# Performance work log

Measured on AMD Instinct MI355X. Metric: run time of the kernel, lower is better.

Reference implementation:

```python
import jax, jax.numpy as jnp
import numpy as np

B, T, IN_DIM = 256, 256, 64
HID, DIM2, OUT_DIM, N_HEADS = 1024, 512, 16, 32


def _linear(x, w, b):
    return x @ w.T + b


def _gru(x, h0, w_ih, w_hh, b_ih, b_hh):
    # x: [B,T,HID], h0: [B,HID]; returns final hidden [B,HID]
    gi_all = jnp.einsum('bti,gi->btg', x, w_ih) + b_ih  # [B,T,3H] precomputed input gates
    def step(h, gi):
        gh = h @ w_hh.T + b_hh
        i_r, i_z, i_n = jnp.split(gi, 3, axis=-1)
        h_r, h_z, h_n = jnp.split(gh, 3, axis=-1)
        r = jax.nn.sigmoid(i_r + h_r)
        z = jax.nn.sigmoid(i_z + h_z)
        n = jnp.tanh(i_n + r * h_n)
        h_new = (1.0 - z) * n + z * h
        return h_new, None
    h, _ = jax.lax.scan(step, h0, jnp.swapaxes(gi_all, 0, 1))
    return h


def setup_inputs() -> dict:
    key = jax.random.key(0)
    ks = jax.random.split(key, 16)
    s = 0.05
    inp = {
        'input': jax.random.normal(ks[0], (B, T, IN_DIM), jnp.float32),
        'hn': jnp.zeros((1, B, HID), jnp.float32),
        'cultivars': jax.random.randint(ks[1], (B, 1), 0, N_HEADS, jnp.int32),
        'fc1_w': jax.random.normal(ks[2], (DIM2, IN_DIM), jnp.float32) * s,
        'fc1_b': jnp.zeros((DIM2,), jnp.float32),
        'fc2_w': jax.random.normal(ks[3], (HID, DIM2), jnp.float32) * s,
        'fc2_b': jnp.zeros((HID,), jnp.float32),
        'w_ih': jax.random.normal(ks[4], (3 * HID, HID), jnp.float32) * s,
        'w_hh': jax.random.normal(ks[5], (3 * HID, HID), jnp.float32) * s,
        'b_ih': jnp.zeros((3 * HID,), jnp.float32),
        'b_hh': jnp.zeros((3 * HID,), jnp.float32),
        'fc3_w': jax.random.normal(ks[6], (DIM2, HID), jnp.float32) * s,
        'fc3_b': jnp.zeros((DIM2,), jnp.float32),
        'heads_w': jax.random.normal(ks[7], (N_HEADS, OUT_DIM, DIM2), jnp.float32) * s,
        'heads_b': jnp.zeros((N_HEADS, OUT_DIM), jnp.float32),
    }
    return inp


def reference(input, hn, cultivars, fc1_w, fc1_b, fc2_w, fc2_b, w_ih, w_hh, b_ih, b_hh, fc3_w, fc3_b, heads_w, heads_b):
    x = _linear(input, fc1_w, fc1_b)          # [B,T,DIM2]
    x = _linear(x, fc2_w, fc2_b)              # [B,T,HID]
    h = _gru(x, hn[0], w_ih, w_hh, b_ih, b_hh)  # [B,HID]
    hn_out = h[None]                          # [1,B,HID]
    out = jax.nn.relu(hn_out)
    out = jax.nn.relu(_linear(out, fc3_w, fc3_b))[0]  # [B,DIM2]
    cidx = cultivars[:, 0]                    # [B]
    w_sel = heads_w[cidx]                     # [B,OUT_DIM,DIM2] gathered head weights
    b_sel = heads_b[cidx]                     # [B,OUT_DIM]
    params = jnp.einsum('bd,bod->bo', out, w_sel) + b_sel
    return params, hn_out
```

## Files before the change

kernel.cpp:

```cpp
#include <hip/hip_runtime.h>

#define T_   256
#define HID_ 1024
#define D2   512

typedef __attribute__((ext_vector_type(8))) short  short8;
typedef __attribute__((ext_vector_type(8))) __bf16 bf16x8;
typedef __attribute__((ext_vector_type(4))) float  f32x4;

__device__ __forceinline__ float sigmoidf_(float x) {
    return __fdividef(1.0f, 1.0f + __expf(-x));
}
__device__ __forceinline__ float tanhf_(float x) {
    return 1.0f - __fdividef(2.0f, 1.0f + __expf(2.0f * x));
}
__device__ __forceinline__ unsigned short bf16hi(float x) {
    unsigned u = __float_as_uint(x);
    return (unsigned short)((u + 0x7FFFu + ((u >> 16) & 1u)) >> 16);
}
__device__ __forceinline__ float bf2f(unsigned short h) {
    return __uint_as_float((unsigned)h << 16);
}
__device__ __forceinline__ f32x4 mfma_(short8 a, short8 b, f32x4 c) {
    union { short8 s; bf16x8 b; } ua, ub;
    ua.s = a; ub.s = b;
    return __builtin_amdgcn_mfma_f32_16x16x32_bf16(ua.b, ub.b, c, 0, 0, 0);
}

__device__ __forceinline__ void gl16(short8& d, const void* p) {
    asm volatile("global_load_dwordx4 %0, %1, off" : "=v"(d) : "v"(p));
}
__device__ __forceinline__ void gl16c(short8& d, const void* p) {
    asm volatile("global_load_dwordx4 %0, %1, off sc0 sc1" : "=v"(d) : "v"(p));
}
__device__ __forceinline__ void gs8c(void* p, unsigned long long v) {
    asm volatile("global_store_dwordx2 %0, %1, off sc0 sc1"
                 :: "v"(p), "v"(v) : "memory");
}
#define WAITV0() asm volatile("s_waitcnt vmcnt(0)" ::: "memory")
#define WAITV8() asm volatile("s_waitcnt vmcnt(8)" ::: "memory")
#define WAITV10_TIE(H, L) asm volatile("s_waitcnt vmcnt(10)" : "+v"(H), "+v"(L) :: "memory")
#define WAITV2_TIE(H, L)  asm volatile("s_waitcnt vmcnt(2)"  : "+v"(H), "+v"(L) :: "memory")
#define WAITV0_TIE(H, L)  asm volatile("s_waitcnt vmcnt(0)"  : "+v"(H), "+v"(L) :: "memory")
#define ABAR() asm volatile("s_waitcnt lgkmcnt(0)\n\ts_barrier" ::: "memory")

__global__ __launch_bounds__(256) void k_w2(
    const float* __restrict__ fc2_w, const float* __restrict__ fc1_w,
    const float* __restrict__ fc1_b, const float* __restrict__ fc2_b,
    float* __restrict__ W2, float* __restrict__ b2)
{
    int idx = blockIdx.x * 256 + threadIdx.x;
    int r = idx >> 6, c = idx & 63;
    float acc = 0.f;
    for (int k = 0; k < D2; ++k)
        acc += fc2_w[(size_t)r * D2 + k] * fc1_w[(size_t)k * 64 + c];
    W2[idx] = acc;
    if (c == 0) {
        float a = fc2_b[r];
        for (int k = 0; k < D2; ++k)
            a += fc2_w[(size_t)r * D2 + k] * fc1_b[k];
        b2[r] = a;
    }
}

__global__ __launch_bounds__(256) void k_wc(
    const float* __restrict__ w_ih, const float* __restrict__ W2,
    const float* __restrict__ b2, const float* __restrict__ b_ih,
    unsigned short* __restrict__ wc_hi, unsigned short* __restrict__ wc_lo,
    float* __restrict__ bc)
{
    int idx = blockIdx.x * 256 + threadIdx.x;
    int r = idx >> 6, c = idx & 63;
    float acc = 0.f;
    for (int k = 0; k < HID_; ++k)
        acc += w_ih[(size_t)r * HID_ + k] * W2[(size_t)k * 64 + c];
    unsigned short h = bf16hi(acc);
    wc_hi[idx] = h;
    wc_lo[idx] = bf16hi(acc - bf2f(h));
    if (c == 0) {
        float a = b_ih[r];
        for (int k = 0; k < HID_; ++k)
            a += w_ih[(size_t)r * HID_ + k] * b2[k];
        bc[r] = a;
    }
}

__global__ __launch_bounds__(256) void k_splitw(
    const float* __restrict__ w, unsigned short* __restrict__ hi,
    unsigned short* __restrict__ lo)
{
    int i4 = (blockIdx.x * 256 + threadIdx.x) * 4;
    float4 v = *(const float4*)(w + i4);
    float vv[4] = {v.x, v.y, v.z, v.w};
    unsigned short h4[4], l4[4];
    #pragma unroll
    for (int i = 0; i < 4; ++i) {
        h4[i] = bf16hi(vv[i]);
        l4[i] = bf16hi(vv[i] - bf2f(h4[i]));
    }
    *(unsigned long long*)(hi + i4) =
        (unsigned long long)h4[0] | ((unsigned long long)h4[1] << 16) |
        ((unsigned long long)h4[2] << 32) | ((unsigned long long)h4[3] << 48);
    *(unsigned long long*)(lo + i4) =
        (unsigned long long)l4[0] | ((unsigned long long)l4[1] << 16) |
        ((unsigned long long)l4[2] << 32) | ((unsigned long long)l4[3] << 48);
}

__global__ __launch_bounds__(256) void k_split_h0(
    const float* __restrict__ hn, unsigned short* __restrict__ hi,
    unsigned short* __restrict__ lo)
{
    int gid = blockIdx.x * 256 + threadIdx.x;
    int b = gid >> 7, kseg = gid & 127;
    const float* src = hn + (size_t)b * HID_ + kseg * 8;
    short8 h8, l8;
    #pragma unroll
    for (int i = 0; i < 8; ++i) {
        float v = src[i];
        unsigned short h = bf16hi(v);
        ((short*)&h8)[i] = (short)h;
        ((short*)&l8)[i] = (short)bf16hi(v - bf2f(h));
    }
    size_t off = (size_t)(kseg >> 2) * 8192 + b * 32 + (kseg & 3) * 8;
    *(short8*)(hi + off) = h8;
    *(short8*)(lo + off) = l8;
}

__global__ __launch_bounds__(256, 1) void k_gru(
    const float* __restrict__ input,
    const float* __restrict__ hn,
    const float* __restrict__ b_hh,
    const float* __restrict__ bc,
    const unsigned short* __restrict__ whh_hi,
    const unsigned short* __restrict__ whh_lo,
    const unsigned short* __restrict__ wc_hi,
    const unsigned short* __restrict__ wc_lo,
    unsigned short* __restrict__ hxA_hi, unsigned short* __restrict__ hxA_lo,
    unsigned short* __restrict__ hxB_hi, unsigned short* __restrict__ hxB_lo,
    float* __restrict__ hn_out,
    int* __restrict__ bar)
{
    const int g = blockIdx.x, ct = g & 31, bt = g >> 5;
    const int j0 = ct << 5, b0 = bt << 5;
    const int tid = threadIdx.x, lane = tid & 63, wid = tid >> 6;
    const int mh = wid & 1, kh = wid >> 1;
    const int l15 = lane & 15, quad = lane >> 4;

    __shared__ short smB[36864];
    float* smF = (float*)smB;
    const int SIN_ = 4672, SHN_ = 6784;

    const int t7 = tid & 127, pl = tid >> 7;
    const unsigned short* wsrc = pl ? whh_lo : whh_hi;
    const unsigned short* csrc = pl ? wc_lo : wc_hi;
    const char* wB[3]; const char* cB[3]; int lo_[3];
    #pragma unroll
    for (int i = 0; i < 3; ++i) {
        int sid = t7 + (i << 7);
        int n = sid >> 2, ss = sid & 3;
        int grow = (n >> 5) * HID_ + j0 + (n & 31);
        wB[i] = (const char*)wsrc + (size_t)grow * 2048u + (size_t)ss * 16u;
        cB[i] = (const char*)csrc + (size_t)grow * 128u + (size_t)ss * 16u;
        lo_[i] = (pl * 96 + n) * 32 + ((ss * 8) ^ (((n >> 1) & 3) << 3));
    }
    const int foff = l15 * 32 + ((quad * 8) ^ (((l15 >> 1) & 3) << 3));
    const size_t aoff = (size_t)((b0 + mh * 16 + l15) * 64 + quad * 16);
    const char* aAh = (const char*)hxA_hi + aoff;
    const char* aAl = (const char*)hxA_lo + aoff;
    const char* aBh = (const char*)hxB_hi + aoff;
    const char* aBl = (const char*)hxB_lo + aoff;
    const float* xrow = input + (size_t)(b0 + mh * 16 + l15) * (T_ * 64)
                              + kh * 32 + quad * 8;

    const int gb = tid >> 3, gj4 = (tid & 7) << 2;
    float hreg[4], br[4], bz[4], bni[4], bnh[4];
    #pragma unroll
    for (int i = 0; i < 4; ++i) {
        int j = j0 + gj4 + i;
        hreg[i] = hn[(size_t)(b0 + gb) * HID_ + j];
        br[i]  = bc[j] + b_hh[j];
        bz[i]  = bc[1024 + j] + b_hh[1024 + j];
        bni[i] = bc[2048 + j];
        bnh[i] = b_hh[2048 + j];
    }
    const size_t hoff = (size_t)(ct * 16384 + (b0 + gb) * 64 + gj4 * 2);
    char* sAh = (char*)hxA_hi + hoff; char* sAl = (char*)hxA_lo + hoff;
    char* sBh = (char*)hxB_hi + hoff; char* sBl = (char*)hxB_lo + hoff;
    const int g73 = gb * 73, g33 = gb * 33;

    int* flags = bar + bt * 128;

    short8 bp[2][6];
    short8 ab[3][2];
    f32x4 acc[6], acci[2];

#define GH_CHUNK(RB, AH, AL)                                                  \
  { _Pragma("unroll")                                                         \
    for (int nt = 0; nt < 6; ++nt) {                                          \
        short8 bh_ = *(const short8*)(smB + (RB) + nt * 512 + foff);          \
        short8 bl_ = *(const short8*)(smB + (RB) + 3072 + nt * 512 + foff);   \
        f32x4 v_ = mfma_(AH, bh_, acc[nt]);                                   \
        v_ = mfma_(AH, bl_, v_);                                              \
        v_ = mfma_(AL, bh_, v_);                                              \
        acc[nt] = v_; } }

    #pragma unroll 1
    for (int t = 0; t < 256; ++t) {
        const char* rh = (t & 1) ? aBh : aAh;
        const char* rl = (t & 1) ? aBl : aAl;
        char* wh = (t & 1) ? sAh : sBh;
        char* wl = (t & 1) ? sAl : sBl;

        short8 gp[6];
        #pragma unroll
        for (int j = 0; j < 6; ++j)
            gl16(gp[j], cB[j % 3] + (j / 3) * 64);
        float xv[8];
        *(float4*)&xv[0] = *(const float4*)(xrow + (size_t)t * 64);
        *(float4*)&xv[4] = *(const float4*)(xrow + (size_t)t * 64 + 4);
        short8 xa_hi, xa_lo;
        #pragma unroll
        for (int i = 0; i < 8; ++i) {
            unsigned short h = bf16hi(xv[i]);
            ((short*)&xa_hi)[i] = (short)h;
            ((short*)&xa_lo)[i] = (short)bf16hi(xv[i] - bf2f(h));
        }
        WAITV0();
        #pragma unroll
        for (int j = 0; j < 6; ++j)
            *(short8*)(smB + (j / 3) * 6144 + lo_[j % 3]) = gp[j];
        #pragma unroll
        for (int j = 0; j < 6; ++j)
            gl16(bp[0][j], wB[j % 3] + (size_t)(j / 3) * 64);
        #pragma unroll
        for (int j = 0; j < 6; ++j)
            gl16(bp[1][j], wB[j % 3] + (size_t)(2 + j / 3) * 64);
        ABAR();
        {
            const int rb = kh * 6144;
            #pragma unroll
            for (int nt = 0; nt < 6; ++nt) {
                short8 bh_ = *(const short8*)(smB + rb + nt * 512 + foff);
                short8 bl_ = *(const short8*)(smB + rb + 3072 + nt * 512 + foff);
                f32x4 z = {0.f, 0.f, 0.f, 0.f};
                f32x4 v = mfma_(xa_hi, bh_, z);
                v = mfma_(xa_hi, bl_, v);
                v = mfma_(xa_lo, bh_, v);
                if (nt < 4) { acc[nt] = v; }
                else { acci[nt - 4] = v; acc[nt] = z; }
            }
        }
        if (t > 0 && wid == 0) {
            int fl = (lane < 32)
                ? __hip_atomic_load(flags + lane, __ATOMIC_RELAXED,
                                    __HIP_MEMORY_SCOPE_SYSTEM)
                : t;
            while (__any(fl < t)) {
                __builtin_amdgcn_s_sleep(1);
                fl = (lane < 32)
                    ? __hip_atomic_load(flags + lane, __ATOMIC_RELAXED,
                                        __HIP_MEMORY_SCOPE_SYSTEM)
                    : t;
            }
        }
        ABAR();
        gl16c(ab[0][0], rh + (size_t)kh * 16384);
        gl16c(ab[0][1], rl + (size_t)kh * 16384);
        WAITV8();
        #pragma unroll
        for (int j = 0; j < 6; ++j)
            *(short8*)(smB + (j / 3) * 6144 + lo_[j % 3]) = bp[0][j];
        gl16c(ab[1][0], rh + (size_t)(2 + kh) * 16384);
        gl16c(ab[1][1], rl + (size_t)(2 + kh) * 16384);
        ABAR();
        #pragma unroll
        for (int G = 0; G < 16; ++G) {
            if (G <= 13) {
                #pragma unroll
                for (int j = 0; j < 6; ++j)
                    gl16(bp[G & 1][j],
                         wB[j % 3] + (size_t)(2 * G + 4 + j / 3) * 64);
                gl16c(ab[(G + 2) % 3][0], rh + (size_t)(2 * (G + 2) + kh) * 16384);
                gl16c(ab[(G + 2) % 3][1], rl + (size_t)(2 * (G + 2) + kh) * 16384);
                WAITV10_TIE(ab[G % 3][0], ab[G % 3][1]);
            } else if (G == 14) {
                WAITV2_TIE(ab[2][0], ab[2][1]);
            } else {
                WAITV0_TIE(ab[0][0], ab[0][1]);
            }
            if (G <= 14) {
                #pragma unroll
                for (int j = 0; j < 6; ++j)
                    *(short8*)(smB + ((G + 1) % 3) * 12288 + (j / 3) * 6144
                               + lo_[j % 3]) = bp[(G + 1) & 1][j];
                ABAR();
            }
            GH_CHUNK((G % 3) * 12288 + kh * 6144, ab[G % 3][0], ab[G % 3][1]);
        }
        __syncthreads();
        {
            const int row = mh * 16 + quad * 4;
            #pragma unroll
            for (int nt = 0; nt < 4; ++nt)
                #pragma unroll
                for (int r = 0; r < 4; ++r)
                    smF[kh * 2336 + (row + r) * 73 + nt * 16 + l15] = acc[nt][r];
            #pragma unroll
            for (int jn = 0; jn < 2; ++jn)
                #pragma unroll
                for (int r = 0; r < 4; ++r) {
                    smF[SHN_ + kh * 1056 + (row + r) * 33 + jn * 16 + l15] = acc[4 + jn][r];
                    smF[SIN_ + kh * 1056 + (row + r) * 33 + jn * 16 + l15] = acci[jn][r];
                }
        }
        __syncthreads();
        unsigned short ph4[4], pl4[4];
        #pragma unroll
        for (int i = 0; i < 4; ++i) {
            int cl = gj4 + i;
            float rp = smF[g73 + cl] + smF[2336 + g73 + cl] + br[i];
            float zp = smF[g73 + 32 + cl] + smF[2336 + g73 + 32 + cl] + bz[i];
            float ip = smF[SIN_ + g33 + cl] + smF[SIN_ + 1056 + g33 + cl] + bni[i];
            float hp = smF[SHN_ + g33 + cl] + smF[SHN_ + 1056 + g33 + cl] + bnh[i];
            float rr = sigmoidf_(rp);
            float zz = sigmoidf_(zp);
            float nn = tanhf_(ip + rr * hp);
            float hv = (1.0f - zz) * nn + zz * hreg[i];
            hreg[i] = hv;
            unsigned short hh = bf16hi(hv);
            ph4[i] = hh;
            pl4[i] = bf16hi(hv - bf2f(hh));
        }
        unsigned long long pk_hi =
            (unsigned long long)ph4[0] | ((unsigned long long)ph4[1] << 16) |
            ((unsigned long long)ph4[2] << 32) | ((unsigned long long)ph4[3] << 48);
        unsigned long long pk_lo =
            (unsigned long long)pl4[0] | ((unsigned long long)pl4[1] << 16) |
            ((unsigned long long)pl4[2] << 32) | ((unsigned long long)pl4[3] << 48);
        gs8c(wh, pk_hi);
        gs8c(wl, pk_lo);
        if (t == 255) {
            #pragma unroll
            for (int i = 0; i < 4; ++i)
                hn_out[(size_t)(b0 + gb) * HID_ + j0 + gj4 + i] = hreg[i];
        }
        WAITV0();
        __syncthreads();
        if (t < 255 && tid == 0)
            __hip_atomic_store(flags + ct, t + 1, __ATOMIC_RELAXED,
                               __HIP_MEMORY_SCOPE_SYSTEM);
    }
#undef GH_CHUNK
}

__global__ __launch_bounds__(256) void k_fc3(
    const float* __restrict__ h, const float* __restrict__ fc3_w,
    const float* __restrict__ fc3_b, float* __restrict__ out3)
{
    const int bt = blockIdx.x >> 3;
    const int dt = blockIdx.x & 7;
    const int b0 = bt << 6;
    const int d0 = dt << 6;
    const int tid = threadIdx.x;
    const int tx = tid & 15, ty = tid >> 4;

    __shared__ float sh_h[64][36];
    __shared__ float sh_w[64][36];

    float acc[4][4] = {};
    const int lr = tid >> 3;
    const int lc = (tid & 7) << 2;

    for (int kk = 0; kk < HID_; kk += 32) {
        #pragma unroll
        for (int p = 0; p < 2; ++p) {
            int row = lr + (p << 5);
            float4 v = *(const float4*)(h + (size_t)(b0 + row) * HID_ + kk + lc);
            v.x = fmaxf(v.x, 0.f); v.y = fmaxf(v.y, 0.f);
            v.z = fmaxf(v.z, 0.f); v.w = fmaxf(v.w, 0.f);
            *(float4*)&sh_h[row][lc] = v;
            *(float4*)&sh_w[row][lc] =
                *(const float4*)(fc3_w + (size_t)(d0 + row) * HID_ + kk + lc);
        }
        __syncthreads();
        #pragma unroll
        for (int k = 0; k < 32; ++k) {
            float hv[4], wv[4];
            #pragma unroll
            for (int i = 0; i < 4; ++i) hv[i] = sh_h[ty + (i << 4)][k];
            #pragma unroll
            for (int q = 0; q < 4; ++q) wv[q] = sh_w[tx + (q << 4)][k];
            #pragma unroll
            for (int i = 0; i < 4; ++i)
                #pragma unroll
                for (int q = 0; q < 4; ++q)
                    acc[i][q] += hv[i] * wv[q];
        }
        __syncthreads();
    }
    #pragma unroll
    for (int i = 0; i < 4; ++i) {
        int b = b0 + ty + (i << 4);
        #pragma unroll
        for (int q = 0; q < 4; ++q) {
            int d = d0 + tx + (q << 4);
            out3[(size_t)b * D2 + d] = fmaxf(acc[i][q] + fc3_b[d], 0.f);
        }
    }
}

__global__ __launch_bounds__(256) void k_heads(
    const float* __restrict__ out3, const int* __restrict__ cult,
    const float* __restrict__ hw, const float* __restrict__ hb,
    float* __restrict__ params)
{
    int b = blockIdx.x;
    int o = threadIdx.x >> 4;
    int l = threadIdx.x & 15;
    int cid = cult[b];
    const float* w = hw + ((size_t)cid * 16 + o) * D2;
    const float* x = out3 + (size_t)b * D2;
    float acc = 0.f;
    #pragma unroll
    for (int m = 0; m < 8; ++m) {
        int d4 = (l + (m << 4)) << 2;
        float4 xv = *(const float4*)(x + d4);
        float4 wv = *(const float4*)(w + d4);
        acc += xv.x * wv.x + xv.y * wv.y + xv.z * wv.z + xv.w * wv.w;
    }
    #pragma unroll
    for (int s = 1; s < 16; s <<= 1)
        acc += __shfl_xor(acc, s, 16);
    if (l == 0)
        params[(size_t)b * 16 + o] = acc + hb[(size_t)cid * 16 + o];
}

extern "C" void kernel_launch(void* const* d_in, const int* in_sizes, int n_in,
                              void* d_out, int out_size, void* d_ws, size_t ws_size,
                              hipStream_t stream)
{
    const float* input = (const float*)d_in[0];
    const float* hn    = (const float*)d_in[1];
    const int*   cult  = (const int*)d_in[2];
    const float* fc1_w = (const float*)d_in[3];
    const float* fc1_b = (const float*)d_in[4];
    const float* fc2_w = (const float*)d_in[5];
    const float* fc2_b = (const float*)d_in[6];
    const float* w_ih  = (const float*)d_in[7];
    const float* w_hh  = (const float*)d_in[8];
    const float* b_ih  = (const float*)d_in[9];
    const float* b_hh  = (const float*)d_in[10];
    const float* fc3_w = (const float*)d_in[11];
    const float* fc3_b = (const float*)d_in[12];
    const float* hw    = (const float*)d_in[13];
    const float* hb    = (const float*)d_in[14];
    float* out = (float*)d_out;
    float* hn_out = out + 4096;

    char* ws = (char*)d_ws;
    int*   bar    = (int*)ws;
    float* W2     = (float*)(ws + 4096);
    float* b2     = (float*)(ws + 266240);
    float* bc     = (float*)(ws + 270336);
    unsigned short* whh_hi = (unsigned short*)(ws + 282624);
    unsigned short* whh_lo = (unsigned short*)(ws + 282624 + 6291456);
    unsigned short* wc_hi  = (unsigned short*)(ws + 12865536);
    unsigned short* wc_lo  = (unsigned short*)(ws + 13258752);
    unsigned short* hxA_hi = (unsigned short*)(ws + 13651968);
    unsigned short* hxA_lo = (unsigned short*)(ws + 14176256);
    unsigned short* hxB_hi = (unsigned short*)(ws + 14700544);
    unsigned short* hxB_lo = (unsigned short*)(ws + 15224832);
    float* out3   = (float*)(ws + 15749120);

    hipMemsetAsync(bar, 0, 4096, stream);
    k_w2<<<256, 256, 0, stream>>>(fc2_w, fc1_w, fc1_b, fc2_b, W2, b2);
    k_wc<<<768, 256, 0, stream>>>(w_ih, W2, b2, b_ih, wc_hi, wc_lo, bc);
    k_splitw<<<3072, 256, 0, stream>>>(w_hh, whh_hi, whh_lo);
    k_split_h0<<<128, 256, 0, stream>>>(hn, hxA_hi, hxA_lo);
    k_gru<<<256, 256, 0, stream>>>(input, hn, b_hh, bc,
                                   whh_hi, whh_lo, wc_hi, wc_lo,
                                   hxA_hi, hxA_lo, hxB_hi, hxB_lo,
                                   hn_out, bar);
    k_fc3<<<32, 256, 0, stream>>>(hn_out, fc3_w, fc3_b, out3);
    k_heads<<<256, 256, 0, stream>>>(out3, cult, hw, hb, out);
}
```

Measured before the change: 3.154 ms.

## Stream GRU recurrent weights directly into LDS via global_load_lds

Replaces register-staged weight loads (global load to VGPRs, then ds_write) with direct global-to-LDS loads for both the combined input weights and the W_hh chunks, and reworks the triple-buffer wait/barrier schedule to match. This removes the VGPR staging buffers and the LDS write instructions in the per-timestep hot loop, which cuts register pressure and VALU/LDS issue work. The swizzled LDS layout is now produced by permuting the global source addresses per lane. The vmcnt accounting is subtler and could expose load latency at barriers.

```diff
diff --git a/kernel.cpp b/kernel.cpp
--- a/kernel.cpp
+++ b/kernel.cpp
@@ -27,9 +27,6 @@
     return __builtin_amdgcn_mfma_f32_16x16x32_bf16(ua.b, ub.b, c, 0, 0, 0);
 }
 
-__device__ __forceinline__ void gl16(short8& d, const void* p) {
-    asm volatile("global_load_dwordx4 %0, %1, off" : "=v"(d) : "v"(p));
-}
 __device__ __forceinline__ void gl16c(short8& d, const void* p) {
     asm volatile("global_load_dwordx4 %0, %1, off sc0 sc1" : "=v"(d) : "v"(p));
 }
@@ -37,9 +34,13 @@
     asm volatile("global_store_dwordx2 %0, %1, off sc0 sc1"
                  :: "v"(p), "v"(v) : "memory");
 }
-#define WAITV0() asm volatile("s_waitcnt vmcnt(0)" ::: "memory")
-#define WAITV8() asm volatile("s_waitcnt vmcnt(8)" ::: "memory")
-#define WAITV10_TIE(H, L) asm volatile("s_waitcnt vmcnt(10)" : "+v"(H), "+v"(L) :: "memory")
+__device__ __forceinline__ void glds16(const void* g, void* l) {
+    __builtin_amdgcn_global_load_lds(
+        (const __attribute__((address_space(1))) unsigned int*)g,
+        (__attribute__((address_space(3))) unsigned int*)l, 16, 0, 0);
+}
+#define WAITV0()  asm volatile("s_waitcnt vmcnt(0)" ::: "memory")
+#define WAITVN6() asm volatile("s_waitcnt vmcnt(6)" ::: "memory")
 #define WAITV2_TIE(H, L)  asm volatile("s_waitcnt vmcnt(2)"  : "+v"(H), "+v"(L) :: "memory")
 #define WAITV0_TIE(H, L)  asm volatile("s_waitcnt vmcnt(0)"  : "+v"(H), "+v"(L) :: "memory")
 #define ABAR() asm volatile("s_waitcnt lgkmcnt(0)\n\ts_barrier" ::: "memory")
@@ -150,18 +151,24 @@
     float* smF = (float*)smB;
     const int SIN_ = 4672, SHN_ = 6784;
 
-    const int t7 = tid & 127, pl = tid >> 7;
-    const unsigned short* wsrc = pl ? whh_lo : whh_hi;
-    const unsigned short* csrc = pl ? wc_lo : wc_hi;
-    const char* wB[3]; const char* cB[3]; int lo_[3];
-    #pragma unroll
-    for (int i = 0; i < 3; ++i) {
-        int sid = t7 + (i << 7);
-        int n = sid >> 2, ss = sid & 3;
+    const char* wsp[6];
+    const char* csp[6];
+    int ldsp[6];
+    #pragma unroll
+    for (int jj = 0; jj < 6; ++jj) {
+        int js  = wid * 6 + jj;
+        int cg  = js / 12;
+        int s12 = js % 12;
+        int rowg = s12 * 16 + (lane >> 2);
+        int q   = lane & 3;
+        int ss  = q ^ ((rowg >> 1) & 3);
+        int pln = rowg / 96, n = rowg % 96;
         int grow = (n >> 5) * HID_ + j0 + (n & 31);
-        wB[i] = (const char*)wsrc + (size_t)grow * 2048u + (size_t)ss * 16u;
-        cB[i] = (const char*)csrc + (size_t)grow * 128u + (size_t)ss * 16u;
-        lo_[i] = (pl * 96 + n) * 32 + ((ss * 8) ^ (((n >> 1) & 3) << 3));
+        wsp[jj] = (const char*)(pln ? whh_lo : whh_hi)
+                + (size_t)grow * 2048u + (size_t)(ss * 16 + cg * 64);
+        csp[jj] = (const char*)(pln ? wc_lo : wc_hi)
+                + (size_t)grow * 128u + (size_t)(ss * 16 + cg * 64);
+        ldsp[jj] = __builtin_amdgcn_readfirstlane(js * 512);
     }
     const int foff = l15 * 32 + ((quad * 8) ^ (((l15 >> 1) & 3) << 3));
     const size_t aoff = (size_t)((b0 + mh * 16 + l15) * 64 + quad * 16);
@@ -190,10 +197,14 @@
 
     int* flags = bar + bt * 128;
 
-    short8 bp[2][6];
     short8 ab[3][2];
     f32x4 acc[6], acci[2];
 
+#define ISSUE_WLDS(BUF, GG)                                                   \
+  { _Pragma("unroll")                                                         \
+    for (int jj_ = 0; jj_ < 6; ++jj_)                                         \
+        glds16(wsp[jj_] + (size_t)(GG) * 128u,                                \
+               (short*)smB + (BUF) * 12288 + ldsp[jj_]); }
 #define GH_CHUNK(RB, AH, AL)                                                  \
   { _Pragma("unroll")                                                         \
     for (int nt = 0; nt < 6; ++nt) {                                          \
@@ -211,10 +222,6 @@
         char* wh = (t & 1) ? sAh : sBh;
         char* wl = (t & 1) ? sAl : sBl;
 
-        short8 gp[6];
-        #pragma unroll
-        for (int j = 0; j < 6; ++j)
-            gl16(gp[j], cB[j % 3] + (j / 3) * 64);
         float xv[8];
         *(float4*)&xv[0] = *(const float4*)(xrow + (size_t)t * 64);
         *(float4*)&xv[4] = *(const float4*)(xrow + (size_t)t * 64 + 4);
@@ -225,16 +232,11 @@
             ((short*)&xa_hi)[i] = (short)h;
             ((short*)&xa_lo)[i] = (short)bf16hi(xv[i] - bf2f(h));
         }
-        WAITV0();
-        #pragma unroll
-        for (int j = 0; j < 6; ++j)
-            *(short8*)(smB + (j / 3) * 6144 + lo_[j % 3]) = gp[j];
-        #pragma unroll
-        for (int j = 0; j < 6; ++j)
-            gl16(bp[0][j], wB[j % 3] + (size_t)(j / 3) * 64);
-        #pragma unroll
-        for (int j = 0; j < 6; ++j)
-            gl16(bp[1][j], wB[j % 3] + (size_t)(2 + j / 3) * 64);
+        #pragma unroll
+        for (int jj = 0; jj < 6; ++jj)
+            glds16(csp[jj], (short*)smB + ldsp[jj]);
+        ISSUE_WLDS(1, 1);
+        WAITVN6();
         ABAR();
         {
             const int rb = kh * 6144;
@@ -264,36 +266,25 @@
             }
         }
         ABAR();
+        ISSUE_WLDS(0, 0);
         gl16c(ab[0][0], rh + (size_t)kh * 16384);
         gl16c(ab[0][1], rl + (size_t)kh * 16384);
-        WAITV8();
-        #pragma unroll
-        for (int j = 0; j < 6; ++j)
-            *(short8*)(smB + (j / 3) * 6144 + lo_[j % 3]) = bp[0][j];
         gl16c(ab[1][0], rh + (size_t)(2 + kh) * 16384);
         gl16c(ab[1][1], rl + (size_t)(2 + kh) * 16384);
+        WAITV2_TIE(ab[0][0], ab[0][1]);
         ABAR();
         #pragma unroll
         for (int G = 0; G < 16; ++G) {
+            if (G >= 1 && G <= 14) {
+                WAITV2_TIE(ab[G % 3][0], ab[G % 3][1]);
+                ABAR();
+            } else if (G == 15) {
+                WAITV0_TIE(ab[0][0], ab[0][1]);
+            }
             if (G <= 13) {
-                #pragma unroll
-                for (int j = 0; j < 6; ++j)
-                    gl16(bp[G & 1][j],
-                         wB[j % 3] + (size_t)(2 * G + 4 + j / 3) * 64);
+                ISSUE_WLDS((G + 2) % 3, G + 2);
                 gl16c(ab[(G + 2) % 3][0], rh + (size_t)(2 * (G + 2) + kh) * 16384);
                 gl16c(ab[(G + 2) % 3][1], rl + (size_t)(2 * (G + 2) + kh) * 16384);
-                WAITV10_TIE(ab[G % 3][0], ab[G % 3][1]);
-            } else if (G == 14) {
-                WAITV2_TIE(ab[2][0], ab[2][1]);
-            } else {
-                WAITV0_TIE(ab[0][0], ab[0][1]);
-            }
-            if (G <= 14) {
-                #pragma unroll
-                for (int j = 0; j < 6; ++j)
-                    *(short8*)(smB + ((G + 1) % 3) * 12288 + (j / 3) * 6144
-                               + lo_[j % 3]) = bp[(G + 1) & 1][j];
-                ABAR();
             }
             GH_CHUNK((G % 3) * 12288 + kh * 6144, ab[G % 3][0], ab[G % 3][1]);
         }
@@ -351,6 +342,7 @@
                                __HIP_MEMORY_SCOPE_SYSTEM);
     }
 #undef GH_CHUNK
+#undef ISSUE_WLDS
 }
 
 __global__ __launch_bounds__(256) void k_fc3(
```

After: 3.341 ms. 1.06x slower.

## Split GRU MFMA work by N-tile instead of M-half per wave

Applied to the files above, without the earlier changes.

Each wave now covers both 16-row batch halves and half of the N tiles (ntg), where before it covered one M half and all six N tiles. Every B fragment read from LDS now feeds two MFMAs, which halves LDS traffic per MFMA. In exchange each wave loads twice as many A (hidden-state) fragments from global memory per chunk, using offset loads. Wait counts are adjusted for the larger number of loads in flight.

```diff
diff --git a/kernel.cpp b/kernel.cpp
--- a/kernel.cpp
+++ b/kernel.cpp
@@ -33,15 +33,22 @@
 __device__ __forceinline__ void gl16c(short8& d, const void* p) {
     asm volatile("global_load_dwordx4 %0, %1, off sc0 sc1" : "=v"(d) : "v"(p));
 }
+__device__ __forceinline__ void gl16c_o(short8& d, const void* p) {
+    asm volatile("global_load_dwordx4 %0, %1, off offset:1024 sc0 sc1"
+                 : "=v"(d) : "v"(p));
+}
 __device__ __forceinline__ void gs8c(void* p, unsigned long long v) {
     asm volatile("global_store_dwordx2 %0, %1, off sc0 sc1"
                  :: "v"(p), "v"(v) : "memory");
 }
-#define WAITV0() asm volatile("s_waitcnt vmcnt(0)" ::: "memory")
-#define WAITV8() asm volatile("s_waitcnt vmcnt(8)" ::: "memory")
-#define WAITV10_TIE(H, L) asm volatile("s_waitcnt vmcnt(10)" : "+v"(H), "+v"(L) :: "memory")
-#define WAITV2_TIE(H, L)  asm volatile("s_waitcnt vmcnt(2)"  : "+v"(H), "+v"(L) :: "memory")
-#define WAITV0_TIE(H, L)  asm volatile("s_waitcnt vmcnt(0)"  : "+v"(H), "+v"(L) :: "memory")
+#define WAITV0()  asm volatile("s_waitcnt vmcnt(0)"  ::: "memory")
+#define WAITV10() asm volatile("s_waitcnt vmcnt(10)" ::: "memory")
+#define WAITV14_T(A,B,C,D) asm volatile("s_waitcnt vmcnt(14)" \
+    : "+v"(A), "+v"(B), "+v"(C), "+v"(D) :: "memory")
+#define WAITV4_T(A,B,C,D)  asm volatile("s_waitcnt vmcnt(4)"  \
+    : "+v"(A), "+v"(B), "+v"(C), "+v"(D) :: "memory")
+#define WAITV0_T(A,B,C,D)  asm volatile("s_waitcnt vmcnt(0)"  \
+    : "+v"(A), "+v"(B), "+v"(C), "+v"(D) :: "memory")
 #define ABAR() asm volatile("s_waitcnt lgkmcnt(0)\n\ts_barrier" ::: "memory")
 
 __global__ __launch_bounds__(256) void k_w2(
@@ -143,7 +150,7 @@
     const int g = blockIdx.x, ct = g & 31, bt = g >> 5;
     const int j0 = ct << 5, b0 = bt << 5;
     const int tid = threadIdx.x, lane = tid & 63, wid = tid >> 6;
-    const int mh = wid & 1, kh = wid >> 1;
+    const int ntg = wid & 1, kh = wid >> 1;
     const int l15 = lane & 15, quad = lane >> 4;
 
     __shared__ short smB[36864];
@@ -164,13 +171,14 @@
         lo_[i] = (pl * 96 + n) * 32 + ((ss * 8) ^ (((n >> 1) & 3) << 3));
     }
     const int foff = l15 * 32 + ((quad * 8) ^ (((l15 >> 1) & 3) << 3));
-    const size_t aoff = (size_t)((b0 + mh * 16 + l15) * 64 + quad * 16);
+    const size_t aoff = (size_t)((b0 + l15) * 64 + quad * 16);
     const char* aAh = (const char*)hxA_hi + aoff;
     const char* aAl = (const char*)hxA_lo + aoff;
     const char* aBh = (const char*)hxB_hi + aoff;
     const char* aBl = (const char*)hxB_lo + aoff;
-    const float* xrow = input + (size_t)(b0 + mh * 16 + l15) * (T_ * 64)
-                              + kh * 32 + quad * 8;
+    const float* xrow0 = input + (size_t)(b0 + l15) * (T_ * 64)
+                               + kh * 32 + quad * 8;
+    const float* xrow1 = xrow0 + (size_t)16 * (T_ * 64);
 
     const int gb = tid >> 3, gj4 = (tid & 7) << 2;
     float hreg[4], br[4], bz[4], bni[4], bnh[4];
@@ -191,18 +199,28 @@
     int* flags = bar + bt * 128;
 
     short8 bp[2][6];
-    short8 ab[3][2];
-    f32x4 acc[6], acci[2];
-
-#define GH_CHUNK(RB, AH, AL)                                                  \
+    short8 ab[3][2][2];
+    f32x4 acc[2][3];
+    f32x4 acci[2];
+
+#define ISSUE_A(BK, C)                                                        \
+  { gl16c  (ab[BK][0][0], rh + (size_t)(C) * 16384);                          \
+    gl16c_o(ab[BK][1][0], rh + (size_t)(C) * 16384);                          \
+    gl16c  (ab[BK][0][1], rl + (size_t)(C) * 16384);                          \
+    gl16c_o(ab[BK][1][1], rl + (size_t)(C) * 16384); }
+#define GH_CHUNK(RB, BK)                                                      \
   { _Pragma("unroll")                                                         \
-    for (int nt = 0; nt < 6; ++nt) {                                          \
-        short8 bh_ = *(const short8*)(smB + (RB) + nt * 512 + foff);          \
-        short8 bl_ = *(const short8*)(smB + (RB) + 3072 + nt * 512 + foff);   \
-        f32x4 v_ = mfma_(AH, bh_, acc[nt]);                                   \
-        v_ = mfma_(AH, bl_, v_);                                              \
-        v_ = mfma_(AL, bh_, v_);                                              \
-        acc[nt] = v_; } }
+    for (int i_ = 0; i_ < 3; ++i_) {                                          \
+        const int nt_ = (i_ < 2) ? (ntg * 2 + i_) : (4 + ntg);                \
+        short8 bh_ = *(const short8*)(smB + (RB) + nt_ * 512 + foff);         \
+        short8 bl_ = *(const short8*)(smB + (RB) + 3072 + nt_ * 512 + foff);  \
+        f32x4 v0_ = mfma_(ab[BK][0][0], bh_, acc[0][i_]);                     \
+        f32x4 v1_ = mfma_(ab[BK][1][0], bh_, acc[1][i_]);                     \
+        v0_ = mfma_(ab[BK][0][0], bl_, v0_);                                  \
+        v1_ = mfma_(ab[BK][1][0], bl_, v1_);                                  \
+        v0_ = mfma_(ab[BK][0][1], bh_, v0_);                                  \
+        v1_ = mfma_(ab[BK][1][1], bh_, v1_);                                  \
+        acc[0][i_] = v0_; acc[1][i_] = v1_; } }
 
     #pragma unroll 1
     for (int t = 0; t < 256; ++t) {
@@ -215,16 +233,20 @@
         #pragma unroll
         for (int j = 0; j < 6; ++j)
             gl16(gp[j], cB[j % 3] + (j / 3) * 64);
-        float xv[8];
-        *(float4*)&xv[0] = *(const float4*)(xrow + (size_t)t * 64);
-        *(float4*)&xv[4] = *(const float4*)(xrow + (size_t)t * 64 + 4);
-        short8 xa_hi, xa_lo;
-        #pragma unroll
-        for (int i = 0; i < 8; ++i) {
-            unsigned short h = bf16hi(xv[i]);
-            ((short*)&xa_hi)[i] = (short)h;
-            ((short*)&xa_lo)[i] = (short)bf16hi(xv[i] - bf2f(h));
-        }
+        float xv[2][8];
+        *(float4*)&xv[0][0] = *(const float4*)(xrow0 + (size_t)t * 64);
+        *(float4*)&xv[0][4] = *(const float4*)(xrow0 + (size_t)t * 64 + 4);
+        *(float4*)&xv[1][0] = *(const float4*)(xrow1 + (size_t)t * 64);
+        *(float4*)&xv[1][4] = *(const float4*)(xrow1 + (size_t)t * 64 + 4);
+        short8 xah[2], xal[2];
+        #pragma unroll
+        for (int m_ = 0; m_ < 2; ++m_)
+            #pragma unroll
+            for (int i = 0; i < 8; ++i) {
+                unsigned short h = bf16hi(xv[m_][i]);
+                ((short*)&xah[m_])[i] = (short)h;
+                ((short*)&xal[m_])[i] = (short)bf16hi(xv[m_][i] - bf2f(h));
+            }
         WAITV0();
         #pragma unroll
         for (int j = 0; j < 6; ++j)
@@ -239,15 +261,19 @@
         {
             const int rb = kh * 6144;
             #pragma unroll
-            for (int nt = 0; nt < 6; ++nt) {
-                short8 bh_ = *(const short8*)(smB + rb + nt * 512 + foff);
-                short8 bl_ = *(const short8*)(smB + rb + 3072 + nt * 512 + foff);
-                f32x4 z = {0.f, 0.f, 0.f, 0.f};
-                f32x4 v = mfma_(xa_hi, bh_, z);
-                v = mfma_(xa_hi, bl_, v);
-                v = mfma_(xa_lo, bh_, v);
-                if (nt < 4) { acc[nt] = v; }
-                else { acci[nt - 4] = v; acc[nt] = z; }
+            for (int i_ = 0; i_ < 3; ++i_) {
+                const int nt_ = (i_ < 2) ? (ntg * 2 + i_) : (4 + ntg);
+                short8 bh_ = *(const short8*)(smB + rb + nt_ * 512 + foff);
+                short8 bl_ = *(const short8*)(smB + rb + 3072 + nt_ * 512 + foff);
+                #pragma unroll
+                for (int m_ = 0; m_ < 2; ++m_) {
+                    f32x4 z = {0.f, 0.f, 0.f, 0.f};
+                    f32x4 v = mfma_(xah[m_], bh_, z);
+                    v = mfma_(xah[m_], bl_, v);
+                    v = mfma_(xal[m_], bh_, v);
+                    if (i_ < 2) { acc[m_][i_] = v; }
+                    else { acci[m_] = v; acc[m_][2] = z; }
+                }
             }
         }
         if (t > 0 && wid == 0) {
@@ -264,14 +290,12 @@
             }
         }
         ABAR();
-        gl16c(ab[0][0], rh + (size_t)kh * 16384);
-        gl16c(ab[0][1], rl + (size_t)kh * 16384);
-        WAITV8();
+        ISSUE_A(0, kh);
+        WAITV10();
         #pragma unroll
         for (int j = 0; j < 6; ++j)
             *(short8*)(smB + (j / 3) * 6144 + lo_[j % 3]) = bp[0][j];
-        gl16c(ab[1][0], rh + (size_t)(2 + kh) * 16384);
-        gl16c(ab[1][1], rl + (size_t)(2 + kh) * 16384);
+        ISSUE_A(1, 2 + kh);
         ABAR();
         #pragma unroll
         for (int G = 0; G < 16; ++G) {
@@ -280,13 +304,13 @@
                 for (int j = 0; j < 6; ++j)
                     gl16(bp[G & 1][j],
                          wB[j % 3] + (size_t)(2 * G + 4 + j / 3) * 64);
-                gl16c(ab[(G + 2) % 3][0], rh + (size_t)(2 * (G + 2) + kh) * 16384);
-                gl16c(ab[(G + 2) % 3][1], rl + (size_t)(2 * (G + 2) + kh) * 16384);
-                WAITV10_TIE(ab[G % 3][0], ab[G % 3][1]);
+                ISSUE_A((G + 2) % 3, 2 * (G + 2) + kh);
+                WAITV14_T(ab[G % 3][0][0], ab[G % 3][0][1],
+                          ab[G % 3][1][0], ab[G % 3][1][1]);
             } else if (G == 14) {
-                WAITV2_TIE(ab[2][0], ab[2][1]);
+                WAITV4_T(ab[2][0][0], ab[2][0][1], ab[2][1][0], ab[2][1][1]);
             } else {
-                WAITV0_TIE(ab[0][0], ab[0][1]);
+                WAITV0_T(ab[0][0][0], ab[0][0][1], ab[0][1][0], ab[0][1][1]);
             }
             if (G <= 14) {
                 #pragma unroll
@@ -295,23 +319,29 @@
                                + lo_[j % 3]) = bp[(G + 1) & 1][j];
                 ABAR();
             }
-            GH_CHUNK((G % 3) * 12288 + kh * 6144, ab[G % 3][0], ab[G % 3][1]);
+            GH_CHUNK((G % 3) * 12288 + kh * 6144, G % 3);
         }
         __syncthreads();
         {
-            const int row = mh * 16 + quad * 4;
-            #pragma unroll
-            for (int nt = 0; nt < 4; ++nt)
+            const int r0 = quad * 4;
+            #pragma unroll
+            for (int m_ = 0; m_ < 2; ++m_) {
                 #pragma unroll
-                for (int r = 0; r < 4; ++r)
-                    smF[kh * 2336 + (row + r) * 73 + nt * 16 + l15] = acc[nt][r];
-            #pragma unroll
-            for (int jn = 0; jn < 2; ++jn)
+                for (int i_ = 0; i_ < 2; ++i_) {
+                    const int nt_ = ntg * 2 + i_;
+                    #pragma unroll
+                    for (int r = 0; r < 4; ++r)
+                        smF[kh * 2336 + (m_ * 16 + r0 + r) * 73 + nt_ * 16 + l15]
+                            = acc[m_][i_][r];
+                }
                 #pragma unroll
                 for (int r = 0; r < 4; ++r) {
-                    smF[SHN_ + kh * 1056 + (row + r) * 33 + jn * 16 + l15] = acc[4 + jn][r];
-                    smF[SIN_ + kh * 1056 + (row + r) * 33 + jn * 16 + l15] = acci[jn][r];
+                    smF[SHN_ + kh * 1056 + (m_ * 16 + r0 + r) * 33 + ntg * 16 + l15]
+                        = acc[m_][2][r];
+                    smF[SIN_ + kh * 1056 + (m_ * 16 + r0 + r) * 33 + ntg * 16 + l15]
+                        = acci[m_][r];
                 }
+            }
         }
         __syncthreads();
         unsigned short ph4[4], pl4[4];
@@ -351,6 +381,7 @@
                                __HIP_MEMORY_SCOPE_SYSTEM);
     }
 #undef GH_CHUNK
+#undef ISSUE_A
 }
 
 __global__ __launch_bounds__(256) void k_fc3(
```

Measured after the change: 3.129 ms. Within noise of the previous version (-0.8%).

## Split GRU recurrence across 512 blocks with 16-column hidden tiles

Applied to the files above, without the earlier changes.

The persistent GRU kernel now gives each block 16 hidden columns instead of 32, doubling the grid to 512 blocks. Shared memory, register tiles, store width and the per-step flag barrier are resized to match, with 64 flags per batch tile and occupancy hint 2. The aim is to halve the per-block MFMA and weight-streaming work on the serial critical path of each timestep by using more CUs. In exchange, each step's inter-block barrier now waits on twice as many producers, the A-operand (h) reloads double in aggregate, and all 512 blocks must be co-resident or the spin-wait deadlocks.

```diff
diff --git a/kernel.cpp b/kernel.cpp
--- a/kernel.cpp
+++ b/kernel.cpp
@@ -33,15 +33,15 @@
 __device__ __forceinline__ void gl16c(short8& d, const void* p) {
     asm volatile("global_load_dwordx4 %0, %1, off sc0 sc1" : "=v"(d) : "v"(p));
 }
-__device__ __forceinline__ void gs8c(void* p, unsigned long long v) {
-    asm volatile("global_store_dwordx2 %0, %1, off sc0 sc1"
+__device__ __forceinline__ void gs4c(void* p, unsigned v) {
+    asm volatile("global_store_dword %0, %1, off sc0 sc1"
                  :: "v"(p), "v"(v) : "memory");
 }
 #define WAITV0() asm volatile("s_waitcnt vmcnt(0)" ::: "memory")
-#define WAITV8() asm volatile("s_waitcnt vmcnt(8)" ::: "memory")
-#define WAITV10_TIE(H, L) asm volatile("s_waitcnt vmcnt(10)" : "+v"(H), "+v"(L) :: "memory")
-#define WAITV2_TIE(H, L)  asm volatile("s_waitcnt vmcnt(2)"  : "+v"(H), "+v"(L) :: "memory")
-#define WAITV0_TIE(H, L)  asm volatile("s_waitcnt vmcnt(0)"  : "+v"(H), "+v"(L) :: "memory")
+#define WAITV5() asm volatile("s_waitcnt vmcnt(5)" ::: "memory")
+#define WAITV7_T(H, L) asm volatile("s_waitcnt vmcnt(7)" : "+v"(H), "+v"(L) :: "memory")
+#define WAITV2_T(H, L) asm volatile("s_waitcnt vmcnt(2)" : "+v"(H), "+v"(L) :: "memory")
+#define WAITV0_T(H, L) asm volatile("s_waitcnt vmcnt(0)" : "+v"(H), "+v"(L) :: "memory")
 #define ABAR() asm volatile("s_waitcnt lgkmcnt(0)\n\ts_barrier" ::: "memory")
 
 __global__ __launch_bounds__(256) void k_w2(
@@ -126,7 +126,7 @@
     *(short8*)(lo + off) = l8;
 }
 
-__global__ __launch_bounds__(256, 1) void k_gru(
+__global__ __launch_bounds__(256, 2) void k_gru(
     const float* __restrict__ input,
     const float* __restrict__ hn,
     const float* __restrict__ b_hh,
@@ -140,28 +140,29 @@
     float* __restrict__ hn_out,
     int* __restrict__ bar)
 {
-    const int g = blockIdx.x, ct = g & 31, bt = g >> 5;
-    const int j0 = ct << 5, b0 = bt << 5;
+    const int g = blockIdx.x, ct = g & 63, bt = g >> 6;
+    const int j0 = ct << 4, b0 = bt << 5;
     const int tid = threadIdx.x, lane = tid & 63, wid = tid >> 6;
     const int mh = wid & 1, kh = wid >> 1;
     const int l15 = lane & 15, quad = lane >> 4;
 
-    __shared__ short smB[36864];
+    __shared__ short smB[18432];
     float* smF = (float*)smB;
-    const int SIN_ = 4672, SHN_ = 6784;
-
-    const int t7 = tid & 127, pl = tid >> 7;
-    const unsigned short* wsrc = pl ? whh_lo : whh_hi;
-    const unsigned short* csrc = pl ? wc_lo : wc_hi;
+    const int SIN_ = 2112, SHN_ = 3200;
+
     const char* wB[3]; const char* cB[3]; int lo_[3];
     #pragma unroll
     for (int i = 0; i < 3; ++i) {
-        int sid = t7 + (i << 7);
-        int n = sid >> 2, ss = sid & 3;
-        int grow = (n >> 5) * HID_ + j0 + (n & 31);
-        wB[i] = (const char*)wsrc + (size_t)grow * 2048u + (size_t)ss * 16u;
-        cB[i] = (const char*)csrc + (size_t)grow * 128u + (size_t)ss * 16u;
-        lo_[i] = (pl * 96 + n) * 32 + ((ss * 8) ^ (((n >> 1) & 3) << 3));
+        int seg = tid + (i << 8);
+        int cg = seg / 384, s = seg % 384;
+        int row = s >> 2, ss = s & 3;
+        int pln = row / 48, n = row % 48;
+        int grow = (n >> 4) * HID_ + j0 + (n & 15);
+        wB[i] = (const char*)(pln ? whh_lo : whh_hi)
+              + (size_t)grow * 2048u + (size_t)(ss * 16 + cg * 64);
+        cB[i] = (const char*)(pln ? wc_lo : wc_hi)
+              + (size_t)grow * 128u + (size_t)(ss * 16 + cg * 64);
+        lo_[i] = cg * 3072 + row * 32 + ((ss * 8) ^ (((row >> 1) & 3) << 3));
     }
     const int foff = l15 * 32 + ((quad * 8) ^ (((l15 >> 1) & 3) << 3));
     const size_t aoff = (size_t)((b0 + mh * 16 + l15) * 64 + quad * 16);
@@ -172,36 +173,42 @@
     const float* xrow = input + (size_t)(b0 + mh * 16 + l15) * (T_ * 64)
                               + kh * 32 + quad * 8;
 
-    const int gb = tid >> 3, gj4 = (tid & 7) << 2;
-    float hreg[4], br[4], bz[4], bni[4], bnh[4];
-    #pragma unroll
-    for (int i = 0; i < 4; ++i) {
-        int j = j0 + gj4 + i;
+    const int gb = tid >> 3, gj2 = (tid & 7) << 1;
+    float hreg[2], br[2], bz[2], bni[2], bnh[2];
+    #pragma unroll
+    for (int i = 0; i < 2; ++i) {
+        int j = j0 + gj2 + i;
         hreg[i] = hn[(size_t)(b0 + gb) * HID_ + j];
         br[i]  = bc[j] + b_hh[j];
         bz[i]  = bc[1024 + j] + b_hh[1024 + j];
         bni[i] = bc[2048 + j];
         bnh[i] = b_hh[2048 + j];
     }
-    const size_t hoff = (size_t)(ct * 16384 + (b0 + gb) * 64 + gj4 * 2);
+    const int j2 = j0 + gj2;
+    const size_t hoff = (size_t)(j2 >> 5) * 16384 + (size_t)(b0 + gb) * 64
+                      + (size_t)((j2 >> 3) & 3) * 16 + (size_t)(j2 & 7) * 2;
     char* sAh = (char*)hxA_hi + hoff; char* sAl = (char*)hxA_lo + hoff;
     char* sBh = (char*)hxB_hi + hoff; char* sBl = (char*)hxB_lo + hoff;
-    const int g73 = gb * 73, g33 = gb * 33;
+    const int g33 = gb * 33, g17 = gb * 17;
 
     int* flags = bar + bt * 128;
 
-    short8 bp[2][6];
+    short8 bp[2][3];
     short8 ab[3][2];
-    f32x4 acc[6], acci[2];
-
-#define GH_CHUNK(RB, AH, AL)                                                  \
-  { _Pragma("unroll")                                                         \
-    for (int nt = 0; nt < 6; ++nt) {                                          \
-        short8 bh_ = *(const short8*)(smB + (RB) + nt * 512 + foff);          \
-        short8 bl_ = *(const short8*)(smB + (RB) + 3072 + nt * 512 + foff);   \
-        f32x4 v_ = mfma_(AH, bh_, acc[nt]);                                   \
-        v_ = mfma_(AH, bl_, v_);                                              \
-        v_ = mfma_(AL, bh_, v_);                                              \
+    f32x4 acc[3];
+    f32x4 acci;
+
+#define ISSUE_A(BK, C)                                                       \
+  { gl16c(ab[BK][0], rh + (size_t)(C) * 16384);                              \
+    gl16c(ab[BK][1], rl + (size_t)(C) * 16384); }
+#define GH_CHUNK(RB, AH, AL)                                                 \
+  { _Pragma("unroll")                                                        \
+    for (int nt = 0; nt < 3; ++nt) {                                         \
+        short8 bh_ = *(const short8*)(smB + (RB) + nt * 512 + foff);         \
+        short8 bl_ = *(const short8*)(smB + (RB) + 1536 + nt * 512 + foff);  \
+        f32x4 v_ = mfma_(AH, bh_, acc[nt]);                                  \
+        v_ = mfma_(AH, bl_, v_);                                             \
+        v_ = mfma_(AL, bh_, v_);                                             \
         acc[nt] = v_; } }
 
     #pragma unroll 1
@@ -211,10 +218,10 @@
         char* wh = (t & 1) ? sAh : sBh;
         char* wl = (t & 1) ? sAl : sBl;
 
-        short8 gp[6];
-        #pragma unroll
-        for (int j = 0; j < 6; ++j)
-            gl16(gp[j], cB[j % 3] + (j / 3) * 64);
+        short8 gp[3];
+        #pragma unroll
+        for (int j = 0; j < 3; ++j)
+            gl16(gp[j], cB[j]);
         float xv[8];
         *(float4*)&xv[0] = *(const float4*)(xrow + (size_t)t * 64);
         *(float4*)&xv[4] = *(const float4*)(xrow + (size_t)t * 64 + 4);
@@ -227,122 +234,108 @@
         }
         WAITV0();
         #pragma unroll
-        for (int j = 0; j < 6; ++j)
-            *(short8*)(smB + (j / 3) * 6144 + lo_[j % 3]) = gp[j];
-        #pragma unroll
-        for (int j = 0; j < 6; ++j)
-            gl16(bp[0][j], wB[j % 3] + (size_t)(j / 3) * 64);
-        #pragma unroll
-        for (int j = 0; j < 6; ++j)
-            gl16(bp[1][j], wB[j % 3] + (size_t)(2 + j / 3) * 64);
+        for (int j = 0; j < 3; ++j)
+            *(short8*)(smB + lo_[j]) = gp[j];
+        #pragma unroll
+        for (int j = 0; j < 3; ++j)
+            gl16(bp[0][j], wB[j]);
+        #pragma unroll
+        for (int j = 0; j < 3; ++j)
+            gl16(bp[1][j], wB[j] + 128);
         ABAR();
         {
-            const int rb = kh * 6144;
-            #pragma unroll
-            for (int nt = 0; nt < 6; ++nt) {
+            const int rb = kh * 3072;
+            #pragma unroll
+            for (int nt = 0; nt < 3; ++nt) {
                 short8 bh_ = *(const short8*)(smB + rb + nt * 512 + foff);
-                short8 bl_ = *(const short8*)(smB + rb + 3072 + nt * 512 + foff);
+                short8 bl_ = *(const short8*)(smB + rb + 1536 + nt * 512 + foff);
                 f32x4 z = {0.f, 0.f, 0.f, 0.f};
                 f32x4 v = mfma_(xa_hi, bh_, z);
                 v = mfma_(xa_hi, bl_, v);
                 v = mfma_(xa_lo, bh_, v);
-                if (nt < 4) { acc[nt] = v; }
-                else { acci[nt - 4] = v; acc[nt] = z; }
+                if (nt < 2) { acc[nt] = v; }
+                else { acci = v; acc[2] = z; }
             }
         }
         if (t > 0 && wid == 0) {
-            int fl = (lane < 32)
-                ? __hip_atomic_load(flags + lane, __ATOMIC_RELAXED,
-                                    __HIP_MEMORY_SCOPE_SYSTEM)
-                : t;
+            int fl = __hip_atomic_load(flags + lane, __ATOMIC_RELAXED,
+                                       __HIP_MEMORY_SCOPE_SYSTEM);
             while (__any(fl < t)) {
                 __builtin_amdgcn_s_sleep(1);
-                fl = (lane < 32)
-                    ? __hip_atomic_load(flags + lane, __ATOMIC_RELAXED,
-                                        __HIP_MEMORY_SCOPE_SYSTEM)
-                    : t;
+                fl = __hip_atomic_load(flags + lane, __ATOMIC_RELAXED,
+                                       __HIP_MEMORY_SCOPE_SYSTEM);
             }
         }
         ABAR();
-        gl16c(ab[0][0], rh + (size_t)kh * 16384);
-        gl16c(ab[0][1], rl + (size_t)kh * 16384);
-        WAITV8();
-        #pragma unroll
-        for (int j = 0; j < 6; ++j)
-            *(short8*)(smB + (j / 3) * 6144 + lo_[j % 3]) = bp[0][j];
-        gl16c(ab[1][0], rh + (size_t)(2 + kh) * 16384);
-        gl16c(ab[1][1], rl + (size_t)(2 + kh) * 16384);
+        ISSUE_A(0, kh);
+        WAITV5();
+        #pragma unroll
+        for (int j = 0; j < 3; ++j)
+            *(short8*)(smB + lo_[j]) = bp[0][j];
+        ISSUE_A(1, 2 + kh);
         ABAR();
         #pragma unroll
         for (int G = 0; G < 16; ++G) {
             if (G <= 13) {
                 #pragma unroll
-                for (int j = 0; j < 6; ++j)
-                    gl16(bp[G & 1][j],
-                         wB[j % 3] + (size_t)(2 * G + 4 + j / 3) * 64);
-                gl16c(ab[(G + 2) % 3][0], rh + (size_t)(2 * (G + 2) + kh) * 16384);
-                gl16c(ab[(G + 2) % 3][1], rl + (size_t)(2 * (G + 2) + kh) * 16384);
-                WAITV10_TIE(ab[G % 3][0], ab[G % 3][1]);
+                for (int j = 0; j < 3; ++j)
+                    gl16(bp[G & 1][j], wB[j] + (size_t)(G + 2) * 128);
+                ISSUE_A((G + 2) % 3, 2 * (G + 2) + kh);
+                WAITV7_T(ab[G % 3][0], ab[G % 3][1]);
             } else if (G == 14) {
-                WAITV2_TIE(ab[2][0], ab[2][1]);
+                WAITV2_T(ab[2][0], ab[2][1]);
             } else {
-                WAITV0_TIE(ab[0][0], ab[0][1]);
+                WAITV0_T(ab[0][0], ab[0][1]);
             }
             if (G <= 14) {
                 #pragma unroll
-                for (int j = 0; j < 6; ++j)
-                    *(short8*)(smB + ((G + 1) % 3) * 12288 + (j / 3) * 6144
-                               + lo_[j % 3]) = bp[(G + 1) & 1][j];
+                for (int j = 0; j < 3; ++j)
+                    *(short8*)(smB + ((G + 1) % 3) * 6144 + lo_[j])
+                        = bp[(G + 1) & 1][j];
                 ABAR();
             }
-            GH_CHUNK((G % 3) * 12288 + kh * 6144, ab[G % 3][0], ab[G % 3][1]);
+            GH_CHUNK((G % 3) * 6144 + kh * 3072, ab[G % 3][0], ab[G % 3][1]);
         }
         __syncthreads();
         {
             const int row = mh * 16 + quad * 4;
             #pragma unroll
-            for (int nt = 0; nt < 4; ++nt)
+            for (int nt = 0; nt < 2; ++nt)
                 #pragma unroll
                 for (int r = 0; r < 4; ++r)
-                    smF[kh * 2336 + (row + r) * 73 + nt * 16 + l15] = acc[nt][r];
-            #pragma unroll
-            for (int jn = 0; jn < 2; ++jn)
-                #pragma unroll
-                for (int r = 0; r < 4; ++r) {
-                    smF[SHN_ + kh * 1056 + (row + r) * 33 + jn * 16 + l15] = acc[4 + jn][r];
-                    smF[SIN_ + kh * 1056 + (row + r) * 33 + jn * 16 + l15] = acci[jn][r];
-                }
+                    smF[kh * 1056 + (row + r) * 33 + nt * 16 + l15] = acc[nt][r];
+            #pragma unroll
+            for (int r = 0; r < 4; ++r) {
+                smF[SHN_ + kh * 544 + (row + r) * 17 + l15] = acc[2][r];
+                smF[SIN_ + kh * 544 + (row + r) * 17 + l15] = acci[r];
+            }
         }
         __syncthreads();
-        unsigned short ph4[4], pl4[4];
-        #pragma unroll
-        for (int i = 0; i < 4; ++i) {
-            int cl = gj4 + i;
-            float rp = smF[g73 + cl] + smF[2336 + g73 + cl] + br[i];
-            float zp = smF[g73 + 32 + cl] + smF[2336 + g73 + 32 + cl] + bz[i];
-            float ip = smF[SIN_ + g33 + cl] + smF[SIN_ + 1056 + g33 + cl] + bni[i];
-            float hp = smF[SHN_ + g33 + cl] + smF[SHN_ + 1056 + g33 + cl] + bnh[i];
+        unsigned short ph2[2], pl2[2];
+        #pragma unroll
+        for (int i = 0; i < 2; ++i) {
+            int cl = gj2 + i;
+            float rp = smF[g33 + cl] + smF[1056 + g33 + cl] + br[i];
+            float zp = smF[g33 + 16 + cl] + smF[1056 + g33 + 16 + cl] + bz[i];
+            float ip = smF[SIN_ + g17 + cl] + smF[SIN_ + 544 + g17 + cl] + bni[i];
+            float hp = smF[SHN_ + g17 + cl] + smF[SHN_ + 544 + g17 + cl] + bnh[i];
             float rr = sigmoidf_(rp);
             float zz = sigmoidf_(zp);
             float nn = tanhf_(ip + rr * hp);
             float hv = (1.0f - zz) * nn + zz * hreg[i];
             hreg[i] = hv;
             unsigned short hh = bf16hi(hv);
-            ph4[i] = hh;
-            pl4[i] = bf16hi(hv - bf2f(hh));
-        }
-        unsigned long long pk_hi =
-            (unsigned long long)ph4[0] | ((unsigned long long)ph4[1] << 16) |
-            ((unsigned long long)ph4[2] << 32) | ((unsigned long long)ph4[3] << 48);
-        unsigned long long pk_lo =
-            (unsigned long long)pl4[0] | ((unsigned long long)pl4[1] << 16) |
-            ((unsigned long long)pl4[2] << 32) | ((unsigned long long)pl4[3] << 48);
-        gs8c(wh, pk_hi);
-        gs8c(wl, pk_lo);
+            ph2[i] = hh;
+            pl2[i] = bf16hi(hv - bf2f(hh));
+        }
+        unsigned pk_hi = (unsigned)ph2[0] | ((unsigned)ph2[1] << 16);
+        unsigned pk_lo = (unsigned)pl2[0] | ((unsigned)pl2[1] << 16);
+        gs4c(wh, pk_hi);
+        gs4c(wl, pk_lo);
         if (t == 255) {
             #pragma unroll
-            for (int i = 0; i < 4; ++i)
-                hn_out[(size_t)(b0 + gb) * HID_ + j0 + gj4 + i] = hreg[i];
+            for (int i = 0; i < 2; ++i)
+                hn_out[(size_t)(b0 + gb) * HID_ + j0 + gj2 + i] = hreg[i];
         }
         WAITV0();
         __syncthreads();
@@ -351,6 +344,7 @@
                                __HIP_MEMORY_SCOPE_SYSTEM);
     }
 #undef GH_CHUNK
+#undef ISSUE_A
 }
 
 __global__ __launch_bounds__(256) void k_fc3(
@@ -477,7 +471,7 @@
     k_wc<<<768, 256, 0, stream>>>(w_ih, W2, b2, b_ih, wc_hi, wc_lo, bc);
     k_splitw<<<3072, 256, 0, stream>>>(w_hh, whh_hi, whh_lo);
     k_split_h0<<<128, 256, 0, stream>>>(hn, hxA_hi, hxA_lo);
-    k_gru<<<256, 256, 0, stream>>>(input, hn, b_hh, bc,
+    k_gru<<<512, 256, 0, stream>>>(input, hn, b_hh, bc,
                                    whh_hi, whh_lo, wc_hi, wc_lo,
                                    hxA_hi, hxA_lo, hxB_hi, hxB_lo,
                                    hn_out, bar);
```

New measurement: 2.598 ms. 1.21x faster.
